# Performance work log

Measured on AMD Instinct MI355X. Metric: run time of the kernel, lower is better.

The kernel has to match this reference:

```python
import jax, jax.numpy as jnp
import numpy as np

N = 10000; E = 320000; NFEAT = 500; NHID = 256; C = 16; K = 64
GAMMA = 4; ALPHA = 0.1; BETA = 1.0; EPS = 0.1; LAMDA = 0.5; W1 = 0.5

def _init(key, shape, scale=0.05):
    return jax.random.normal(key, shape, dtype=jnp.float32) * scale

def setup_inputs():
    key = jax.random.key(0)
    ks = jax.random.split(key, 24)
    return {
        "x": jax.random.normal(ks[0], (N, NFEAT), dtype=jnp.float32),
        "edge_index": jax.random.randint(ks[1], (2, E), 0, N),
        "edge_weight": jax.random.uniform(ks[2], (E,), dtype=jnp.float32),
        "adj_weight": jax.random.uniform(ks[3], (E,), dtype=jnp.float32),
        "connect": jax.random.uniform(ks[4], (N, N), dtype=jnp.float32),
        "confidence_in": jax.random.uniform(ks[5], (2, E), dtype=jnp.float32),
        "lin1_w": _init(ks[6], (NHID, NFEAT)),
        "lin1_b": jnp.zeros((NHID,), jnp.float32),
        "lin2_w": _init(ks[7], (C, NHID)),
        "lin2_b": jnp.zeros((C,), jnp.float32),
        "lin_a_w": _init(ks[8], (NHID, N), 0.01),
        "lin_a_b": jnp.zeros((NHID,), jnp.float32),
        "lin_n_w": _init(ks[9], (C, C)),
        "lin_n_b": jnp.zeros((C,), jnp.float32),
        "left_w": _init(ks[10], (C, C)),
        "att_w": _init(ks[11], (1, C)),
        "v_w": _init(ks[12], (K, NHID)),
        "v_b": jnp.zeros((K,), jnp.float32),
        "W": _init(ks[13], (C, C)),
        "conf_param": jnp.zeros((3,), jnp.float32),
        "b_param": jnp.zeros((1,), jnp.float32),
    }

def _forward(x, edge_index, edge_weight, adj_weight, connect, confidence_in,
             lin1_w, lin1_b, lin2_w, lin2_b, lin_a_w, lin_a_b, lin_n_w, lin_n_b,
             left_w, att_w, v_w, v_b, W, conf_param, b_param):
    row, col = edge_index[0], edge_index[1]

    def spmm(vals, out_idx, M):
        # COO sparse @ dense: scatter-add per-edge vals * gathered rows of M
        return jax.ops.segment_sum(vals[:, None] * M, out_idx, num_segments=N)

    x_a = connect @ lin_a_w.T + lin_a_b            # [N, NHID]
    h = x @ lin1_w.T + lin1_b
    h = jax.nn.relu((1.0 - LAMDA) * h + LAMDA * x_a)
    raw = h                                        # [N, NHID]
    h = h @ lin2_w.T + lin2_b                      # [N, C]

    # neighbor label distribution: row-normalized adj @ one_hot(argmax softmax)
    y_hat = jnp.argmax(jax.nn.softmax(h, axis=1), axis=1)
    one_hot = jax.nn.one_hot(y_hat, C, dtype=h.dtype)
    nei = spmm(adj_weight, row, one_hot[col])
    s = nei.sum(axis=1, keepdims=True)
    nei = jnp.where(s != 0, nei / jnp.where(s == 0, 1.0, s), 0.0)

    x_n = jax.nn.relu(nei @ lin_n_w.T + lin_n_b)
    h = (1.0 - W1) * h + W1 * x_n
    init = h

    # per-edge attention-based confidence mixed with input confidences
    lx = h @ left_w.T
    confi = jax.nn.relu(lx[row] + lx[col])
    confi = jax.nn.sigmoid((confi @ att_w.T)[:, 0])
    w = jax.nn.softmax(conf_param)
    conf = confi * w[0] + confidence_in[0] * w[1] + confidence_in[1] * w[2]  # [E]

    V = raw @ v_w.T + v_b                          # [N, K]
    U = spmm(adj_weight, row, V[col]) @ jnp.linalg.inv(V.T @ V)
    eyeK = jnp.eye(K, dtype=h.dtype)

    def edge_mask_score(score):
        S = score ** 2
        ss = jnp.sort(S)
        q1, q3 = ss[E // 4], ss[3 * E // 4]
        thr = (q3 + 1.5 * (q3 - q1)) * conf        # [E]
        mask = (S < thr).astype(h.dtype)
        return (score + b_param[0]) * mask

    def update_u(U, V):
        SS = edge_mask_score(edge_weight - jnp.sum(U[row] * V[col], axis=1))
        temp = spmm(SS, row, V[col]) + U @ (V.T @ V) + EPS * (h @ (h.T @ V))
        inver = jnp.linalg.inv((1.0 + EPS) * (V.T @ V) + BETA * eyeK)
        return temp @ inver

    def update_v(U, V):
        SS = edge_mask_score(edge_weight - jnp.sum(V[row] * U[col], axis=1))
        # A^T @ U: scatter over col with U[row]
        temp = spmm(SS, col, U[row]) + V @ (U.T @ U) + EPS * (h @ (h.T @ U))
        inver = jnp.linalg.inv((1.0 + EPS) * (U.T @ U) + BETA * eyeK)
        return temp @ inver

    for j in range(GAMMA):
        if j % 2 == 0:
            U = update_u(U, V)
        else:
            V = update_v(U, V)

    prop = U @ (h.T @ V).T                         # [N, C]
    out = (1.0 - ALPHA) * prop + ALPHA * init
    return out @ W

def reference(x, edge_index, edge_weight, adj_weight, connect, confidence_in,
              lin1_w, lin1_b, lin2_w, lin2_b, lin_a_w, lin_a_b, lin_n_w, lin_n_b,
              left_w, att_w, v_w, v_b, W, conf_param, b_param):
    return _forward(x, edge_index, edge_weight, adj_weight, connect, confidence_in,
                    lin1_w, lin1_b, lin2_w, lin2_b, lin_a_w, lin_a_b, lin_n_w, lin_n_b,
                    left_w, att_w, v_w, v_b, W, conf_param, b_param)
```

## Files before the change

### kernel.cpp

```cpp
#include <hip/hip_runtime.h>
#include <cstddef>
#include <cstdint>


constexpr int kN  = 10000;
constexpr int kE  = 320000;
constexpr int kNH = 256;
constexpr int kC  = 16;
constexpr int kK  = 64;
constexpr int GRAM_PARTS = 256;
constexpr int PHASE_BLOCKS = 768;

struct SelState {
  int bin1[2]; int rem1[2];
};

typedef short bf16x8 __attribute__((ext_vector_type(8)));
typedef float f32x4 __attribute__((ext_vector_type(4)));
typedef ushort ushort8 __attribute__((ext_vector_type(8)));

__device__ __forceinline__ ushort f2bf(float x) {
  unsigned u = __float_as_uint(x);
  unsigned r = (u + 0x7fffu + ((u >> 16) & 1u)) >> 16;
  return (ushort)r;
}
__device__ __forceinline__ float bf2f(ushort h) {
  return __uint_as_float((unsigned)h << 16);
}
__device__ __forceinline__ int swz(int row, int byteInRow) {
  int chunk = (byteInRow >> 4) ^ ((row >> 1) & 3);
  return row * 64 + (chunk << 4) + (byteInRow & 15);
}

__global__ void split3_bf(const float* __restrict__ Wa, ushort* ha, ushort* la,
                          const float* __restrict__ Wx, ushort* hx, ushort* lx2,
                          const float* __restrict__ Wv, ushort* hv, ushort* lv)
{
  const int n1 = 256 * 10016, n2 = 256 * 512, n3 = 64 * 256;
  int t = blockIdx.x * 256 + threadIdx.x;
  if (t < n1) {
    int r = t / 10016, c = t % 10016;
    float v = (c < 10000) ? Wa[(size_t)r * 10000 + c] : 0.f;
    ushort h = f2bf(v); ha[t] = h; la[t] = f2bf(v - bf2f(h));
  } else if (t < n1 + n2) {
    int q = t - n1;
    int r = q / 512, c = q % 512;
    float v = (c < 500) ? Wx[(size_t)r * 500 + c] : 0.f;
    ushort h = f2bf(v); hx[q] = h; lx2[q] = f2bf(v - bf2f(h));
  } else if (t < n1 + n2 + n3) {
    int q = t - n1 - n2;
    float v = Wv[q];
    ushort h = f2bf(v); hv[q] = h; lv[q] = f2bf(v - bf2f(h));
  }
}

template<int BN, bool ALO>
__global__ __launch_bounds__(256) void gemm_v3(
    const float* __restrict__ A, const ushort* __restrict__ Bhg,
    const ushort* __restrict__ Blg, const float* __restrict__ bias,
    float* __restrict__ out, int M, int K, int Kp, int KR, int outStride)
{
  __shared__ __align__(16) char sAh[64 * 64];
  __shared__ __align__(16) char sAl[ALO ? 64 * 64 : 16];
  __shared__ __align__(16) char sBh[BN * 64];
  __shared__ __align__(16) char sBl[BN * 64];
  const int t = threadIdx.x;
  const int lane = t & 63, w = t >> 6;
  const int bm = blockIdx.x * 64;
  const int k0 = blockIdx.z * KR;
  const int kend = min(K, k0 + KR);
  out += (size_t)blockIdx.z * M * outStride;
  constexpr int WN = BN / 64;
  constexpr int RB = WN;
  const int wc = (w % WN) * 64;
  const int wr = (w / WN) * (RB * 16);
  const int l15 = lane & 15;
  const int lByte = (lane >> 4) * 16;
  const int ar = t >> 2, ac = t & 3;

  f32x4 acc[RB][4] = {};
  for (int kt = k0; kt < kend; kt += 32) {
    {
      int gr = bm + ar, gk = kt + ac * 8;
      float v[8];
      if (gr < M && gk + 8 <= kend) {
        float4 v0 = *reinterpret_cast<const float4*>(A + (size_t)gr * K + gk);
        float4 v1 = *reinterpret_cast<const float4*>(A + (size_t)gr * K + gk + 4);
        v[0] = v0.x; v[1] = v0.y; v[2] = v0.z; v[3] = v0.w;
        v[4] = v1.x; v[5] = v1.y; v[6] = v1.z; v[7] = v1.w;
      } else {
#pragma unroll
        for (int q = 0; q < 8; q++)
          v[q] = (gr < M && gk + q < kend) ? A[(size_t)gr * K + gk + q] : 0.f;
      }
      ushort8 h8, l8;
#pragma unroll
      for (int q = 0; q < 8; q++) {
        ushort h = f2bf(v[q]); h8[q] = h;
        if (ALO) l8[q] = f2bf(v[q] - bf2f(h));
      }
      *reinterpret_cast<ushort8*>(sAh + swz(ar, ac * 16)) = h8;
      if (ALO) *reinterpret_cast<ushort8*>(sAl + swz(ar, ac * 16)) = l8;
    }
#pragma unroll
    for (int i2 = 0; i2 < BN / 64; i2++) {
      int idx = t + i2 * 256;
      int r = idx >> 2, c = idx & 3;
      size_t gb = (size_t)r * Kp + kt + c * 8;
      ushort8 hv = *reinterpret_cast<const ushort8*>(Bhg + gb);
      ushort8 lv = *reinterpret_cast<const ushort8*>(Blg + gb);
      *reinterpret_cast<ushort8*>(sBh + swz(r, c * 16)) = hv;
      *reinterpret_cast<ushort8*>(sBl + swz(r, c * 16)) = lv;
    }
    __syncthreads();
    bf16x8 bh[4], bl[4];
#pragma unroll
    for (int nbq = 0; nbq < 4; nbq++) {
      int rr = wc + nbq * 16 + l15;
      bh[nbq] = *reinterpret_cast<const bf16x8*>(sBh + swz(rr, lByte));
      bl[nbq] = *reinterpret_cast<const bf16x8*>(sBl + swz(rr, lByte));
    }
#pragma unroll
    for (int rb = 0; rb < RB; rb++) {
      int rr = wr + rb * 16 + l15;
      bf16x8 ah = *reinterpret_cast<const bf16x8*>(sAh + swz(rr, lByte));
#pragma unroll
      for (int nbq = 0; nbq < 4; nbq++) {
        acc[rb][nbq] = __builtin_amdgcn_mfma_f32_16x16x32_bf16(ah, bh[nbq], acc[rb][nbq], 0, 0, 0);
        acc[rb][nbq] = __builtin_amdgcn_mfma_f32_16x16x32_bf16(ah, bl[nbq], acc[rb][nbq], 0, 0, 0);
      }
      if (ALO) {
        bf16x8 al = *reinterpret_cast<const bf16x8*>(sAl + swz(rr, lByte));
#pragma unroll
        for (int nbq = 0; nbq < 4; nbq++)
          acc[rb][nbq] = __builtin_amdgcn_mfma_f32_16x16x32_bf16(al, bh[nbq], acc[rb][nbq], 0, 0, 0);
      }
    }
    __syncthreads();
  }
#pragma unroll
  for (int rb = 0; rb < RB; rb++) {
#pragma unroll
    for (int nbq = 0; nbq < 4; nbq++) {
      int colg = wc + nbq * 16 + l15;
      float bv = bias ? bias[colg] : 0.f;
#pragma unroll
      for (int jj = 0; jj < 4; jj++) {
        int rowg = bm + wr + rb * 16 + (lane >> 4) * 4 + jj;
        if (rowg < M) out[(size_t)rowg * outStride + colg] = acc[rb][nbq][jj] + bv;
      }
    }
  }
}

__global__ void reduce_raw(const float4* __restrict__ Pa, const float4* px,
                           const float* __restrict__ ba, const float* __restrict__ b1,
                           float4* rawOut, int* cntR, int* cntC, int* fillR,
                           int* fillC, float* nei)
{
  int t = blockIdx.x * 256 + threadIdx.x;
  if (t < kN) { cntR[t] = 0; cntC[t] = 0; fillR[t] = 0; fillC[t] = 0; }
  if (t < kN * kC) nei[t] = 0.f;
  if (t >= kN * kNH / 4) return;
  const int sl = kN * kNH / 4;
  float4 s = Pa[t];
#pragma unroll
  for (int p = 1; p < 6; p++) {
    float4 q = Pa[t + (size_t)p * sl];
    s.x += q.x; s.y += q.y; s.z += q.z; s.w += q.w;
  }
  float4 pxv = px[t];
  int c4 = t & 63;
  float4 vba = reinterpret_cast<const float4*>(ba)[c4];
  float4 vb1 = reinterpret_cast<const float4*>(b1)[c4];
  float4 r;
  r.x = fmaxf(0.5f * (s.x + vba.x) + 0.5f * (pxv.x + vb1.x), 0.f);
  r.y = fmaxf(0.5f * (s.y + vba.y) + 0.5f * (pxv.y + vb1.y), 0.f);
  r.z = fmaxf(0.5f * (s.z + vba.z) + 0.5f * (pxv.z + vb1.z), 0.f);
  r.w = fmaxf(0.5f * (s.w + vba.w) + 0.5f * (pxv.w + vb1.w), 0.f);
  rawOut[t] = r;
}

struct MegaArgs {
  const float* raw;
  const float* lin2_w; const float* lin2_b;
  const int* row; const int* col;
  const float* aw; const float* ew;
  const float* lnw; const float* lnb;
  const float* left_w; const float* att_w;
  const float* ci; const float* conf_p; const float* b_param;
  const float* Wm;
  float* h16; int* yhat; float* nei; float* hC; float* lx; float* conf;
  int* cntR; int* cntC; int* fillR; int* fillC; int* startR; int* startC;
  int* eR; int* eC; int* othR; int* othC;
  float* Va; float* Vb; float* Ua; float* Ub; float* T;
  float* score; float* G; float* Gi; float* Gp; float* hTX; float* Hp;
  int* hist1; int* h2a; int* h2b;
  int* hist1C; int* h2aC; int* h2bC;
  float* P;
  SelState* sel;
  float* out;
};

__device__ __forceinline__ void uv_at(const MegaArgs& a, int j,
                                      float*& Ucur, float*& Unxt,
                                      float*& Vcur, float*& Vnxt)
{
  int uU = (j >= 1) + (j >= 3);
  int uV = (j >= 2) + (j >= 4);
  Ucur = (uU & 1) ? a.Ub : a.Ua; Unxt = (uU & 1) ? a.Ua : a.Ub;
  Vcur = (uV & 1) ? a.Vb : a.Va; Vnxt = (uV & 1) ? a.Va : a.Vb;
}

__device__ void gram2_dev(const float* M, const float* hc, float* P, int b, float* shm)
{
  float* sM = shm;
  float* sH = shm + 512;
  const int t = threadIdx.x;
  const int aG = t >> 2, cG0 = (t & 3) * 16;
  const int aH = t >> 4, cH0 = (t & 15) * 4;
  float accG[16]; float accH[4];
#pragma unroll
  for (int q = 0; q < 16; q++) accG[q] = 0.f;
#pragma unroll
  for (int q = 0; q < 4; q++) accH[q] = 0.f;
  int r0 = b * 40, r1 = min(kN, r0 + 40);
  for (int rb = r0; rb < r1; rb += 8) {
    int nb2 = min(8, r1 - rb);
    __syncthreads();
    for (int q = t; q < nb2 * 64; q += 256) sM[q] = M[(size_t)rb * 64 + q];
    for (int q = t; q < nb2 * 16; q += 256) sH[q] = hc[(size_t)rb * 16 + q];
    __syncthreads();
    for (int r = 0; r < nb2; r++) {
      float avG = sM[r * 64 + aG];
      const float* sbG = &sM[r * 64 + cG0];
#pragma unroll
      for (int q = 0; q < 16; q++) accG[q] += avG * sbG[q];
      float avH = sH[r * 16 + aH];
      const float* sbH = &sM[r * 64 + cH0];
#pragma unroll
      for (int q = 0; q < 4; q++) accH[q] += avH * sbH[q];
    }
  }
  float* p1 = P + (size_t)b * 5120 + aG * 64 + cG0;
#pragma unroll
  for (int q = 0; q < 16; q++) p1[q] = accG[q];
  float* p2 = P + (size_t)b * 5120 + 4096 + aH * 64 + cH0;
#pragma unroll
  for (int q = 0; q < 4; q++) p2[q] = accH[q];
}

__device__ void inverse_dev(const float* G, float* Gi, float alpha, float beta,
                            const float* hTX, float* Gp, float* Hp, float* shm)
{
  float* A = shm;
  float* prow = shm + 8448;
  float* fcol = shm + 8576;
  const int t = threadIdx.x;
  for (int q = t; q < 64 * 128; q += 256) {
    int r = q >> 7, c = q & 127;
    float v;
    if (c < 64) v = alpha * G[r * 64 + c] + ((c == r) ? beta : 0.f);
    else        v = (c - 64 == r) ? 1.f : 0.f;
    A[r * 132 + c] = v;
  }
  __syncthreads();
  const int i  = t >> 2;
  const int c0 = (t & 3) * 32;
  for (int k = 0; k < 64; k++) {
    if (t < 128) prow[t] = A[k * 132 + t];
    else if (t < 192) fcol[t - 128] = A[(t - 128) * 132 + k];
    __syncthreads();
    float pinv = 1.f / prow[k];
    float f = fcol[i];
    float4* Ar = reinterpret_cast<float4*>(&A[i * 132 + c0]);
    const float4* pr = reinterpret_cast<const float4*>(&prow[c0]);
    if (i == k) {
#pragma unroll
      for (int q = 0; q < 8; q++) {
        float4 p = pr[q];
        p.x *= pinv; p.y *= pinv; p.z *= pinv; p.w *= pinv;
        Ar[q] = p;
      }
    } else {
#pragma unroll
      for (int q = 0; q < 8; q++) {
        float4 p = pr[q]; float4 av = Ar[q];
        av.x -= f * (p.x * pinv); av.y -= f * (p.y * pinv);
        av.z -= f * (p.z * pinv); av.w -= f * (p.w * pinv);
        Ar[q] = av;
      }
    }
    __syncthreads();
  }
  for (int q = t; q < 4096; q += 256) Gi[q] = A[(q >> 6) * 132 + 64 + (q & 63)];
  if (Gp) {
    for (int q = t; q < 4096; q += 256) {
      int r = q >> 6, k = q & 63;
      float s = 0.f;
#pragma unroll 8
      for (int jj = 0; jj < 64; jj++) s += G[r * 64 + jj] * A[jj * 132 + 64 + k];
      Gp[q] = s;
    }
    for (int q = t; q < 1024; q += 256) {
      int c = q >> 6, k = q & 63;
      float s = 0.f;
#pragma unroll 8
      for (int jj = 0; jj < 64; jj++) s += hTX[c * 64 + jj] * A[jj * 132 + 64 + k];
      Hp[q] = 0.1f * s;
    }
  }
}

__device__ void hscan(const int* __restrict__ Hc, const int* __restrict__ Hf,
                      int R, int* shm, int outSlot)
{
  const int t = threadIdx.x;
  int* part = shm;
  int c = Hc[t];
  __syncthreads();
  part[t] = c;
  __syncthreads();
  for (int off = 1; off < 256; off <<= 1) {
    int v = part[t];
    int u = (t >= off) ? part[t - off] : 0;
    __syncthreads();
    part[t] = v + u;
    __syncthreads();
  }
  int cum = part[t] - c;
  if (R >= cum && R < cum + c) { shm[outSlot + 2] = t; shm[outSlot + 3] = R - cum; }
  __syncthreads();
  int cb = shm[outSlot + 2], rem = shm[outSlot + 3];
  int f = Hf[cb * 256 + t];
  __syncthreads();
  part[t] = f;
  __syncthreads();
  for (int off = 1; off < 256; off <<= 1) {
    int v = part[t];
    int u = (t >= off) ? part[t - off] : 0;
    __syncthreads();
    part[t] = v + u;
    __syncthreads();
  }
  int cum2 = part[t] - f;
  if (rem >= cum2 && rem < cum2 + f) { shm[outSlot] = cb * 256 + t; shm[outSlot + 1] = rem - cum2; }
  __syncthreads();
}

__device__ void spmm_dev(const float* vals, const float* score, const float* conf,
                         float thr, float bp0,
                         const int* start, const int* eids, const int* oth,
                         const float* Msrc, float* T, int wid0, int wstride)
{
  int lane = threadIdx.x & 63;
  for (int wid = wid0; wid < kN; wid += wstride) {
    int p = start[wid], pend = start[wid + 1];
    float acc = 0.f;
    for (; p + 4 <= pend; p += 4) {
      int e0 = eids[p], e1 = eids[p + 1], e2 = eids[p + 2], e3 = eids[p + 3];
      int o0 = oth[p], o1 = oth[p + 1], o2 = oth[p + 2], o3 = oth[p + 3];
      float m0 = Msrc[(size_t)o0 * 64 + lane];
      float m1 = Msrc[(size_t)o1 * 64 + lane];
      float m2 = Msrc[(size_t)o2 * 64 + lane];
      float m3 = Msrc[(size_t)o3 * 64 + lane];
      float v0, v1, v2, v3;
      if (vals) { v0 = vals[e0]; v1 = vals[e1]; v2 = vals[e2]; v3 = vals[e3]; }
      else {
        float s0 = score[e0], s1 = score[e1], s2 = score[e2], s3 = score[e3];
        v0 = (s0 * s0 < thr * conf[e0]) ? (s0 + bp0) : 0.f;
        v1 = (s1 * s1 < thr * conf[e1]) ? (s1 + bp0) : 0.f;
        v2 = (s2 * s2 < thr * conf[e2]) ? (s2 + bp0) : 0.f;
        v3 = (s3 * s3 < thr * conf[e3]) ? (s3 + bp0) : 0.f;
      }
      acc += v0 * m0 + v1 * m1 + v2 * m2 + v3 * m3;
    }
    for (; p < pend; ++p) {
      int e = eids[p];
      float v;
      if (vals) v = vals[e];
      else { float sc = score[e]; v = (sc * sc < thr * conf[e]) ? (sc + bp0) : 0.f; }
      acc += v * Msrc[(size_t)oth[p] * 64 + lane];
    }
    T[(size_t)wid * 64 + lane] = acc;
  }
}

__device__ void outf_dev(const MegaArgs& a, const float* T, const float* X,
                         float* Out, int gtid, int gsz)
{
  for (int i = gtid; i < 65536; i += gsz) { a.hist1[i] = 0; a.h2a[i] = 0; a.h2b[i] = 0; }
  if (gtid < 256) { a.hist1C[gtid] = 0; a.h2aC[gtid] = 0; a.h2bC[gtid] = 0; }
  for (int t = gtid; t < kN * 16; t += gsz) {
    int i = t >> 4, kq = t & 15;
    const float* ti = T + (size_t)i * 64;
    const float4* G4 = reinterpret_cast<const float4*>(a.Gi);
    float4 s = make_float4(0.f, 0.f, 0.f, 0.f);
#pragma unroll 8
    for (int jj = 0; jj < 64; jj++) {
      float tv = ti[jj];
      float4 g = G4[jj * 16 + kq];
      s.x += tv * g.x; s.y += tv * g.y; s.z += tv * g.z; s.w += tv * g.w;
    }
    if (X) {
      const float* xi = X + (size_t)i * 64;
      const float4* Gp4 = reinterpret_cast<const float4*>(a.Gp);
      float4 s2 = make_float4(0.f, 0.f, 0.f, 0.f);
#pragma unroll 8
      for (int jj = 0; jj < 64; jj++) {
        float xv = xi[jj];
        float4 g = Gp4[jj * 16 + kq];
        s2.x += xv * g.x; s2.y += xv * g.y; s2.z += xv * g.z; s2.w += xv * g.w;
      }
      s.x += s2.x; s.y += s2.y; s.z += s2.z; s.w += s2.w;
      const float4* Hp4 = reinterpret_cast<const float4*>(a.Hp);
      float4 s3 = make_float4(0.f, 0.f, 0.f, 0.f);
#pragma unroll
      for (int c = 0; c < 16; c++) {
        float hv = a.hC[(size_t)i * 16 + c];
        float4 g = Hp4[c * 16 + kq];
        s3.x += hv * g.x; s3.y += hv * g.y; s3.z += hv * g.z; s3.w += hv * g.w;
      }
      s.x += s3.x; s.y += s3.y; s.z += s3.z; s.w += s3.w;
    }
    *reinterpret_cast<float4*>(Out + (size_t)i * 64 + kq * 4) = s;
  }
}

__device__ void reduce_dev(const MegaArgs& a, int gtid, int gsz)
{
  for (int c = gtid; c < 5120; c += gsz) {
    float s = 0.f;
    for (int p = 0; p < GRAM_PARTS; p++) s += a.P[(size_t)p * 5120 + c];
    if (c < 4096) a.G[c] = s;
    else a.hTX[c - 4096] = s;
  }
}

__global__ __launch_bounds__(256, 4) void mega_phase(MegaArgs a, int phase, int j)
{
  __shared__ __align__(16) float smem[8704];
  const int tid = threadIdx.x;
  const int bid = blockIdx.x;
  const int nb  = gridDim.x;
  const int gtid = bid * 256 + tid;
  const int gsz = nb * 256;
  float *Ucur, *Unxt, *Vcur, *Vnxt;
  uv_at(a, j, Ucur, Unxt, Vcur, Vnxt);
  bool up = ((j & 1) == 0);
  const float* Ma   = up ? Ucur : Vcur;
  const float* Mb   = up ? Vcur : Ucur;
  const float* Moth = up ? Vcur : Ucur;
  const float* Xcur = up ? Ucur : Vcur;
  float* Xout       = up ? Unxt : Vnxt;

  switch (phase) {
  case 0: {
    for (int t = gtid; t < kN * 16; t += gsz) {
      int i = t >> 4, jj = t & 15;
      const float4* av4 = reinterpret_cast<const float4*>(a.raw + (size_t)i * 256);
      const float4* bv4 = reinterpret_cast<const float4*>(a.lin2_w + (size_t)jj * 256);
      float s = a.lin2_b[jj];
#pragma unroll 8
      for (int q = 0; q < 64; q++) {
        float4 av = av4[q], bv = bv4[q];
        s += av.x * bv.x + av.y * bv.y + av.z * bv.z + av.w * bv.w;
      }
      a.h16[t] = s;
      float m = s; int am = jj;
#pragma unroll
      for (int off = 1; off < 16; off <<= 1) {
        float om = __shfl_xor(m, off);
        int oa = __shfl_xor(am, off);
        if (om > m || (om == m && oa < am)) { m = om; am = oa; }
      }
      if (jj == 0) a.yhat[i] = am;
    }
  } break;
  case 1: {
    for (int e = gtid; e < kE; e += gsz) {
      int r = a.row[e], c = a.col[e];
      atomicAdd(&a.cntR[r], 1);
      atomicAdd(&a.cntC[c], 1);
      atomicAdd(&a.nei[(size_t)r * 16 + a.yhat[c]], a.aw[e]);
    }
    for (int part = bid; part < GRAM_PARTS; part += nb)
      gram2_dev(a.Va, a.Va, a.P, part, smem);
  } break;
  case 2: {
    if (bid == 0) {
      int* part = (int*)smem;
      for (int pass = 0; pass < 2; ++pass) {
        const int* cnt = pass ? a.cntC : a.cntR;
        int* start = pass ? a.startC : a.startR;
        int bbase = tid * 40;
        int s = 0;
        for (int q = 0; q < 40; q++) { int idx = bbase + q; if (idx < kN) s += cnt[idx]; }
        part[tid] = s;
        __syncthreads();
        for (int off = 1; off < 256; off <<= 1) {
          int v = part[tid];
          int u = (tid >= off) ? part[tid - off] : 0;
          __syncthreads();
          part[tid] = v + u;
          __syncthreads();
        }
        int run = part[tid] - s;
        for (int q = 0; q < 40; q++) {
          int idx = bbase + q;
          if (idx < kN) { start[idx] = run; run += cnt[idx]; }
        }
        if (tid == 255) start[kN] = part[255];
        __syncthreads();
      }
    } else {
      int g2 = (bid - 1) * 256 + tid, s2 = (nb - 1) * 256;
      for (int i = g2; i < kN; i += s2) {
        float nv[16]; float s = 0.f;
#pragma unroll
        for (int c = 0; c < 16; c++) { nv[c] = a.nei[(size_t)i * 16 + c]; s += nv[c]; }
        float inv = (s != 0.f) ? 1.f / s : 0.f;
#pragma unroll
        for (int jj = 0; jj < 16; jj++) {
          float xn = a.lnb[jj];
#pragma unroll
          for (int c = 0; c < 16; c++) xn += (nv[c] * inv) * a.lnw[jj * 16 + c];
          xn = fmaxf(xn, 0.f);
          a.hC[(size_t)i * 16 + jj] = 0.5f * a.h16[(size_t)i * 16 + jj] + 0.5f * xn;
        }
      }
      for (int c = g2; c < 5120; c += s2) {
        float s = 0.f;
        for (int p = 0; p < GRAM_PARTS; p++) s += a.P[(size_t)p * 5120 + c];
        if (c < 4096) a.G[c] = s;
        else a.hTX[c - 4096] = s;
      }
    }
  } break;
  case 3: {
    if (bid == 0) {
      inverse_dev(a.G, a.Gi, 1.0f, 0.0f, nullptr, nullptr, nullptr, smem);
    } else {
      int g2 = (bid - 1) * 256 + tid, s2 = (nb - 1) * 256;
      for (int e = g2; e < kE; e += s2) {
        int r = a.row[e], c = a.col[e];
        int pr = a.startR[r] + atomicAdd(&a.fillR[r], 1);
        a.eR[pr] = e; a.othR[pr] = c;
        int pc = a.startC[c] + atomicAdd(&a.fillC[c], 1);
        a.eC[pc] = e; a.othC[pc] = r;
      }
      for (int t = g2; t < kN * 16; t += s2) {
        int i = t >> 4, jj = t & 15;
        float s = 0.f;
#pragma unroll
        for (int c = 0; c < 16; c++) s += a.hC[(size_t)i * 16 + c] * a.left_w[jj * 16 + c];
        a.lx[t] = s;
      }
    }
  } break;
  case 4: {
    for (int e = gtid; e < kE; e += gsz) {
      float p0 = a.conf_p[0], p1 = a.conf_p[1], p2 = a.conf_p[2];
      float m = fmaxf(p0, fmaxf(p1, p2));
      float e0 = expf(p0 - m), e1 = expf(p1 - m), e2 = expf(p2 - m);
      float inv = 1.f / (e0 + e1 + e2);
      float w0 = e0 * inv, w1 = e1 * inv, w2 = e2 * inv;
      const float* aa = a.lx + (size_t)a.row[e] * 16;
      const float* bb = a.lx + (size_t)a.col[e] * 16;
      float s = 0.f;
#pragma unroll
      for (int c = 0; c < 16; c++) s += fmaxf(aa[c] + bb[c], 0.f) * a.att_w[c];
      float cf = 1.f / (1.f + expf(-s));
      a.conf[e] = cf * w0 + a.ci[e] * w1 + a.ci[(size_t)kE + e] * w2;
    }
    spmm_dev(a.aw, nullptr, nullptr, 0.f, 0.f,
             a.startR, a.eR, a.othR, a.Va, a.T, bid * 4 + (tid >> 6), nb * 4);
  } break;
  case 5: outf_dev(a, a.T, nullptr, a.Ua, gtid, gsz); break;
  case 6: {
    int* lh = (int*)smem;
    lh[tid] = 0;
    __syncthreads();
    for (int e = gtid; e < kE; e += gsz) {
      const float4* av4 = reinterpret_cast<const float4*>(Ma + (size_t)a.row[e] * 64);
      const float4* bv4 = reinterpret_cast<const float4*>(Mb + (size_t)a.col[e] * 64);
      float s = 0.f;
#pragma unroll
      for (int q = 0; q < 16; q++) {
        float4 av = av4[q], bv = bv4[q];
        s += av.x * bv.x + av.y * bv.y + av.z * bv.z + av.w * bv.w;
      }
      float sc = a.ew[e] - s;
      a.score[e] = sc;
      unsigned u = __float_as_uint(sc * sc);
      atomicAdd(&a.hist1[u >> 16], 1);
      atomicAdd(&lh[u >> 24], 1);
    }
    __syncthreads();
    if (lh[tid] > 0) atomicAdd(&a.hist1C[tid], lh[tid]);
    for (int part = bid; part < GRAM_PARTS; part += nb)
      gram2_dev(Moth, a.hC, a.P, part, smem);
  } break;
  case 7: {
    reduce_dev(a, gtid, gsz);
    int* ishm = (int*)smem;
    hscan(a.hist1C, a.hist1, kE / 4, ishm, 260);
    int b0 = ishm[260];
    if (bid == 0 && tid == 0) { a.sel->bin1[0] = ishm[260]; a.sel->rem1[0] = ishm[261]; }
    hscan(a.hist1C, a.hist1, 3 * kE / 4, ishm, 264);
    int b1 = ishm[264];
    if (bid == 0 && tid == 0) { a.sel->bin1[1] = ishm[264]; a.sel->rem1[1] = ishm[265]; }
    __syncthreads();
    int* lhA = ishm + 512;
    int* lhB = ishm + 768;
    lhA[tid] = 0; lhB[tid] = 0;
    __syncthreads();
    for (int e = gtid; e < kE; e += gsz) {
      float sc = a.score[e];
      unsigned u = __float_as_uint(sc * sc);
      int top = (int)(u >> 16);
      if (top == b0) { atomicAdd(&a.h2a[u & 0xFFFF], 1); atomicAdd(&lhA[(u >> 8) & 0xFF], 1); }
      if (top == b1) { atomicAdd(&a.h2b[u & 0xFFFF], 1); atomicAdd(&lhB[(u >> 8) & 0xFF], 1); }
    }
    __syncthreads();
    if (lhA[tid] > 0) atomicAdd(&a.h2aC[tid], lhA[tid]);
    if (lhB[tid] > 0) atomicAdd(&a.h2bC[tid], lhB[tid]);
  } break;
  case 8: {
    if (bid == 0) {
      inverse_dev(a.G, a.Gi, 1.1f, 1.0f, a.hTX, a.Gp, a.Hp, smem);
    } else {
      int* ishm = (int*)smem;
      int bA = a.sel->bin1[0], bB = a.sel->bin1[1];
      int rA = a.sel->rem1[0], rB = a.sel->rem1[1];
      hscan(a.h2aC, a.h2a, rA, ishm, 260);
      int f0 = ishm[260];
      hscan(a.h2bC, a.h2b, rB, ishm, 264);
      int f1 = ishm[264];
      float q1 = __uint_as_float(((unsigned)bA << 16) | (unsigned)f0);
      float q3 = __uint_as_float(((unsigned)bB << 16) | (unsigned)f1);
      float thr = q3 + 1.5f * (q3 - q1);
      float bp0 = a.b_param[0];
      if (up) spmm_dev(nullptr, a.score, a.conf, thr, bp0,
                       a.startR, a.eR, a.othR, Vcur, a.T,
                       (bid - 1) * 4 + (tid >> 6), (nb - 1) * 4);
      else    spmm_dev(nullptr, a.score, a.conf, thr, bp0,
                       a.startC, a.eC, a.othC, Ucur, a.T,
                       (bid - 1) * 4 + (tid >> 6), (nb - 1) * 4);
    }
  } break;
  case 9: outf_dev(a, a.T, Xcur, Xout, gtid, gsz); break;
  case 10: {
    for (int part = bid; part < GRAM_PARTS; part += nb)
      gram2_dev(Vcur, a.hC, a.P, part, smem);
  } break;
  case 11: reduce_dev(a, gtid, gsz); break;
  case 12: {
    float* sh = smem;
    float* sW = smem + 1024;
    for (int q = tid; q < 1024; q += 256) sh[q] = a.hTX[q];
    sW[tid] = a.Wm[tid & 255];
    __syncthreads();
    for (int i = gtid; i < kN; i += gsz) {
      const float* u = Ucur + (size_t)i * 64;
      float pre[16];
#pragma unroll
      for (int c = 0; c < 16; c++) {
        float s = 0.f;
#pragma unroll
        for (int k = 0; k < 64; k++) s += u[k] * sh[c * 64 + k];
        pre[c] = 0.9f * s + 0.1f * a.hC[(size_t)i * 16 + c];
      }
#pragma unroll
      for (int jj = 0; jj < 16; jj++) {
        float o = 0.f;
#pragma unroll
        for (int c = 0; c < 16; c++) o += pre[c] * sW[c * 16 + jj];
        a.out[(size_t)i * 16 + jj] = o;
      }
    }
  } break;
  }
}

extern "C" void kernel_launch(void* const* d_in, const int* in_sizes, int n_in,
                              void* d_out, int out_size, void* d_ws, size_t ws_size,
                              hipStream_t stream)
{
  const float* x       = (const float*)d_in[0];
  const int*   eidx    = (const int*)d_in[1];
  const float* ew      = (const float*)d_in[2];
  const float* aw      = (const float*)d_in[3];
  const float* connect = (const float*)d_in[4];
  const float* ci      = (const float*)d_in[5];
  const float* lin1_w  = (const float*)d_in[6];
  const float* lin1_b  = (const float*)d_in[7];
  const float* lin2_w  = (const float*)d_in[8];
  const float* lin2_b  = (const float*)d_in[9];
  const float* lin_a_w = (const float*)d_in[10];
  const float* lin_a_b = (const float*)d_in[11];
  const float* lin_n_w = (const float*)d_in[12];
  const float* lin_n_b = (const float*)d_in[13];
  const float* left_w  = (const float*)d_in[14];
  const float* att_w   = (const float*)d_in[15];
  const float* v_w     = (const float*)d_in[16];
  const float* v_b     = (const float*)d_in[17];
  const float* Wm      = (const float*)d_in[18];
  const float* conf_p  = (const float*)d_in[19];
  const float* b_param = (const float*)d_in[20];
  const int* row = eidx;
  const int* col = eidx + kE;
  float* out = (float*)d_out;

  char* base = (char*)d_ws;
  size_t off = 0;
  auto alloc = [&](size_t bytes) -> void* {
    void* p = base + off;
    off += bytes;
    off = (off + 255) & ~(size_t)255;
    return p;
  };
  float* raw   = (float*)alloc((size_t)kN * kNH * 4);
  float* h16   = (float*)alloc((size_t)kN * kC * 4);
  float* hC    = (float*)alloc((size_t)kN * kC * 4);
  float* nei   = (float*)alloc((size_t)kN * kC * 4);
  float* lx    = (float*)alloc((size_t)kN * kC * 4);
  int*   yhat  = (int*)alloc((size_t)kN * 4);
  float* conf  = (float*)alloc((size_t)kE * 4);
  float* Va    = (float*)alloc((size_t)kN * kK * 4);
  float* Vb    = (float*)alloc((size_t)kN * kK * 4);
  float* Ua    = (float*)alloc((size_t)kN * kK * 4);
  float* Ub    = (float*)alloc((size_t)kN * kK * 4);
  float* T     = (float*)alloc((size_t)kN * kK * 4);
  float* score = (float*)alloc((size_t)kE * 4);
  float* G     = (float*)alloc(64 * 64 * 4);
  float* Gi    = (float*)alloc(64 * 64 * 4);
  float* Gp    = (float*)alloc(64 * 64 * 4);
  float* hTX   = (float*)alloc(kC * kK * 4);
  float* Hp    = (float*)alloc(kC * kK * 4);
  int* hist1   = (int*)alloc(65536 * 4);
  int* h2a     = (int*)alloc(65536 * 4);
  int* h2b     = (int*)alloc(65536 * 4);
  int* hist1C  = (int*)alloc(256 * 4);
  int* h2aC    = (int*)alloc(256 * 4);
  int* h2bC    = (int*)alloc(256 * 4);
  SelState* sel = (SelState*)alloc(sizeof(SelState));
  int* cntR    = (int*)alloc((size_t)kN * 4);
  int* cntC    = (int*)alloc((size_t)kN * 4);
  int* fillR   = (int*)alloc((size_t)kN * 4);
  int* fillC   = (int*)alloc((size_t)kN * 4);
  int* startR  = (int*)alloc((size_t)(kN + 1) * 4);
  int* startC  = (int*)alloc((size_t)(kN + 1) * 4);
  int* eR      = (int*)alloc((size_t)kE * 4);
  int* eC      = (int*)alloc((size_t)kE * 4);
  int* othR    = (int*)alloc((size_t)kE * 4);
  int* othC    = (int*)alloc((size_t)kE * 4);
  float* P     = (float*)alloc((size_t)GRAM_PARTS * 5120 * 4);
  const int KpC = 10016, KpX = 512, KpV = 256;
  ushort* BcH = (ushort*)alloc((size_t)256 * KpC * 2);
  ushort* BcL = (ushort*)alloc((size_t)256 * KpC * 2);
  ushort* BxH = (ushort*)alloc((size_t)256 * KpX * 2);
  ushort* BxL = (ushort*)alloc((size_t)256 * KpX * 2);
  ushort* BvH = (ushort*)alloc((size_t)64 * KpV * 2);
  ushort* BvL = (ushort*)alloc((size_t)64 * KpV * 2);
  float* Pbig  = (float*)alloc((size_t)6 * kN * kNH * 4);

  {
    int total = 256 * KpC + 256 * KpX + 64 * KpV;
    split3_bf<<<(total + 255) / 256, 256, 0, stream>>>(
        lin_a_w, BcH, BcL, lin1_w, BxH, BxL, v_w, BvH, BvL);
  }

  gemm_v3<256, false><<<dim3(157, 1, 6), 256, 0, stream>>>(
      connect, BcH, BcL, nullptr, Pbig, kN, 10000, KpC, 1696, kNH);
  gemm_v3<256, true><<<dim3(157, 1, 1), 256, 0, stream>>>(
      x, BxH, BxL, nullptr, raw, kN, 500, KpX, 512, kNH);
  reduce_raw<<<(kN * kNH / 4 + 255) / 256, 256, 0, stream>>>(
      (const float4*)Pbig, (const float4*)raw, lin_a_b, lin1_b, (float4*)raw,
      cntR, cntC, fillR, fillC, nei);
  gemm_v3<64, true><<<dim3(157, 1, 1), 256, 0, stream>>>(
      raw, BvH, BvL, v_b, Va, kN, 256, KpV, 256, kK);

  MegaArgs ma;
  ma.raw = raw; ma.lin2_w = lin2_w; ma.lin2_b = lin2_b;
  ma.row = row; ma.col = col; ma.aw = aw; ma.ew = ew;
  ma.lnw = lin_n_w; ma.lnb = lin_n_b; ma.left_w = left_w; ma.att_w = att_w;
  ma.ci = ci; ma.conf_p = conf_p; ma.b_param = b_param; ma.Wm = Wm;
  ma.h16 = h16; ma.yhat = yhat; ma.nei = nei; ma.hC = hC; ma.lx = lx; ma.conf = conf;
  ma.cntR = cntR; ma.cntC = cntC; ma.fillR = fillR; ma.fillC = fillC;
  ma.startR = startR; ma.startC = startC;
  ma.eR = eR; ma.eC = eC; ma.othR = othR; ma.othC = othC;
  ma.Va = Va; ma.Vb = Vb; ma.Ua = Ua; ma.Ub = Ub; ma.T = T;
  ma.score = score; ma.G = G; ma.Gi = Gi; ma.Gp = Gp; ma.hTX = hTX; ma.Hp = Hp;
  ma.hist1 = hist1; ma.h2a = h2a; ma.h2b = h2b;
  ma.hist1C = hist1C; ma.h2aC = h2aC; ma.h2bC = h2bC;
  ma.P = P; ma.sel = sel; ma.out = out;

  const dim3 pg(PHASE_BLOCKS);
  for (int p = 0; p <= 5; p++) mega_phase<<<pg, 256, 0, stream>>>(ma, p, 0);
  for (int j = 0; j < 4; j++)
    for (int p = 6; p <= 9; p++) mega_phase<<<pg, 256, 0, stream>>>(ma, p, j);
  mega_phase<<<pg, 256, 0, stream>>>(ma, 10, 4);
  mega_phase<<<pg, 256, 0, stream>>>(ma, 11, 4);
  mega_phase<<<pg, 256, 0, stream>>>(ma, 12, 4);
}
```

Baseline: 2.226 ms.

## Replace coarse histogram with single-block flat scan in new phase

Drops the per-block shared-memory coarse histogram and its global atomics from the score phase. A new phase is inserted in which block 0 scans the full 65536-bin histogram to find the quantile bins, while the other blocks compute the Gram partials that used to run in the score phase. The next phase then reads the selected bins instead of re-scanning in every block. This removes redundant per-block scans but adds one extra kernel launch per iteration and a serial single-block scan.

New measurement: 2.103 ms. -5.5%, faster.

```diff
diff --git a/kernel.cpp b/kernel.cpp
--- a/kernel.cpp
+++ b/kernel.cpp
@@ -196,7 +196,7 @@
   float* Va; float* Vb; float* Ua; float* Ub; float* T;
   float* score; float* G; float* Gi; float* Gp; float* hTX; float* Hp;
   int* hist1; int* h2a; int* h2b;
-  int* hist1C; int* h2aC; int* h2bC;
+  int* h2aC; int* h2bC;
   float* P;
   SelState* sel;
   float* out;
@@ -309,6 +309,39 @@
       for (int jj = 0; jj < 64; jj++) s += hTX[c * 64 + jj] * A[jj * 132 + 64 + k];
       Hp[q] = 0.1f * s;
     }
+  }
+}
+
+__device__ void flat_scan1(const int* __restrict__ H, SelState* sel, int* shm)
+{
+  const int t = threadIdx.x;
+  int* part = shm;
+  for (int tgt = 0; tgt < 2; tgt++) {
+    const int4* H4 = reinterpret_cast<const int4*>(H + t * 256);
+    int R = tgt ? (3 * kE / 4) : (kE / 4);
+    int lsum = 0;
+    for (int b = 0; b < 64; b++) { int4 v = H4[b]; lsum += v.x + v.y + v.z + v.w; }
+    part[t] = lsum;
+    __syncthreads();
+    for (int off = 1; off < 256; off <<= 1) {
+      int v = part[t];
+      int u = (t >= off) ? part[t - off] : 0;
+      __syncthreads();
+      part[t] = v + u;
+      __syncthreads();
+    }
+    int cum = part[t] - lsum;
+    int fb = -1, fr = 0;
+    for (int b = 0; b < 64; b++) {
+      int4 v = H4[b];
+      int bb = t * 256 + b * 4;
+      if (fb < 0 && R >= cum && R < cum + v.x) { fb = bb;     fr = R - cum; } cum += v.x;
+      if (fb < 0 && R >= cum && R < cum + v.y) { fb = bb + 1; fr = R - cum; } cum += v.y;
+      if (fb < 0 && R >= cum && R < cum + v.z) { fb = bb + 2; fr = R - cum; } cum += v.z;
+      if (fb < 0 && R >= cum && R < cum + v.w) { fb = bb + 3; fr = R - cum; } cum += v.w;
+    }
+    if (fb >= 0) { sel->bin1[tgt] = fb; sel->rem1[tgt] = fr; }
+    __syncthreads();
   }
 }
 
@@ -390,7 +423,7 @@
                          float* Out, int gtid, int gsz)
 {
   for (int i = gtid; i < 65536; i += gsz) { a.hist1[i] = 0; a.h2a[i] = 0; a.h2b[i] = 0; }
-  if (gtid < 256) { a.hist1C[gtid] = 0; a.h2aC[gtid] = 0; a.h2bC[gtid] = 0; }
+  if (gtid < 256) { a.h2aC[gtid] = 0; a.h2bC[gtid] = 0; }
   for (int t = gtid; t < kN * 16; t += gsz) {
     int i = t >> 4, kq = t & 15;
     const float* ti = T + (size_t)i * 64;
@@ -578,9 +611,6 @@
   } break;
   case 5: outf_dev(a, a.T, nullptr, a.Ua, gtid, gsz); break;
   case 6: {
-    int* lh = (int*)smem;
-    lh[tid] = 0;
-    __syncthreads();
     for (int e = gtid; e < kE; e += gsz) {
       const float4* av4 = reinterpret_cast<const float4*>(Ma + (size_t)a.row[e] * 64);
       const float4* bv4 = reinterpret_cast<const float4*>(Mb + (size_t)a.col[e] * 64);
@@ -594,25 +624,18 @@
       a.score[e] = sc;
       unsigned u = __float_as_uint(sc * sc);
       atomicAdd(&a.hist1[u >> 16], 1);
-      atomicAdd(&lh[u >> 24], 1);
-    }
-    __syncthreads();
-    if (lh[tid] > 0) atomicAdd(&a.hist1C[tid], lh[tid]);
-    for (int part = bid; part < GRAM_PARTS; part += nb)
+    }
+  } break;
+  case 7: {
+    if (bid == 0) flat_scan1(a.hist1, a.sel, (int*)smem);
+    else for (int part = bid - 1; part < GRAM_PARTS; part += nb - 1)
       gram2_dev(Moth, a.hC, a.P, part, smem);
   } break;
-  case 7: {
+  case 8: {
     reduce_dev(a, gtid, gsz);
-    int* ishm = (int*)smem;
-    hscan(a.hist1C, a.hist1, kE / 4, ishm, 260);
-    int b0 = ishm[260];
-    if (bid == 0 && tid == 0) { a.sel->bin1[0] = ishm[260]; a.sel->rem1[0] = ishm[261]; }
-    hscan(a.hist1C, a.hist1, 3 * kE / 4, ishm, 264);
-    int b1 = ishm[264];
-    if (bid == 0 && tid == 0) { a.sel->bin1[1] = ishm[264]; a.sel->rem1[1] = ishm[265]; }
-    __syncthreads();
-    int* lhA = ishm + 512;
-    int* lhB = ishm + 768;
+    int b0 = a.sel->bin1[0], b1 = a.sel->bin1[1];
+    int* lhA = (int*)smem;
+    int* lhB = (int*)smem + 256;
     lhA[tid] = 0; lhB[tid] = 0;
     __syncthreads();
     for (int e = gtid; e < kE; e += gsz) {
@@ -626,7 +649,7 @@
     if (lhA[tid] > 0) atomicAdd(&a.h2aC[tid], lhA[tid]);
     if (lhB[tid] > 0) atomicAdd(&a.h2bC[tid], lhB[tid]);
   } break;
-  case 8: {
+  case 9: {
     if (bid == 0) {
       inverse_dev(a.G, a.Gi, 1.1f, 1.0f, a.hTX, a.Gp, a.Hp, smem);
     } else {
@@ -649,13 +672,13 @@
                        (bid - 1) * 4 + (tid >> 6), (nb - 1) * 4);
     }
   } break;
-  case 9: outf_dev(a, a.T, Xcur, Xout, gtid, gsz); break;
-  case 10: {
+  case 10: outf_dev(a, a.T, Xcur, Xout, gtid, gsz); break;
+  case 11: {
     for (int part = bid; part < GRAM_PARTS; part += nb)
       gram2_dev(Vcur, a.hC, a.P, part, smem);
   } break;
-  case 11: reduce_dev(a, gtid, gsz); break;
-  case 12: {
+  case 12: reduce_dev(a, gtid, gsz); break;
+  case 13: {
     float* sh = smem;
     float* sW = smem + 1024;
     for (int q = tid; q < 1024; q += 256) sh[q] = a.hTX[q];
@@ -741,7 +764,6 @@
   int* hist1   = (int*)alloc(65536 * 4);
   int* h2a     = (int*)alloc(65536 * 4);
   int* h2b     = (int*)alloc(65536 * 4);
-  int* hist1C  = (int*)alloc(256 * 4);
   int* h2aC    = (int*)alloc(256 * 4);
   int* h2bC    = (int*)alloc(256 * 4);
   SelState* sel = (SelState*)alloc(sizeof(SelState));
@@ -793,14 +815,14 @@
   ma.Va = Va; ma.Vb = Vb; ma.Ua = Ua; ma.Ub = Ub; ma.T = T;
   ma.score = score; ma.G = G; ma.Gi = Gi; ma.Gp = Gp; ma.hTX = hTX; ma.Hp = Hp;
   ma.hist1 = hist1; ma.h2a = h2a; ma.h2b = h2b;
-  ma.hist1C = hist1C; ma.h2aC = h2aC; ma.h2bC = h2bC;
+  ma.h2aC = h2aC; ma.h2bC = h2bC;
   ma.P = P; ma.sel = sel; ma.out = out;
 
   const dim3 pg(PHASE_BLOCKS);
   for (int p = 0; p <= 5; p++) mega_phase<<<pg, 256, 0, stream>>>(ma, p, 0);
   for (int j = 0; j < 4; j++)
-    for (int p = 6; p <= 9; p++) mega_phase<<<pg, 256, 0, stream>>>(ma, p, j);
-  mega_phase<<<pg, 256, 0, stream>>>(ma, 10, 4);
+    for (int p = 6; p <= 10; p++) mega_phase<<<pg, 256, 0, stream>>>(ma, p, j);
   mega_phase<<<pg, 256, 0, stream>>>(ma, 11, 4);
   mega_phase<<<pg, 256, 0, stream>>>(ma, 12, 4);
-}
+  mega_phase<<<pg, 256, 0, stream>>>(ma, 13, 4);
+}
```
